# Kernel optimization log

Hardware: AMD Instinct MI355X
Metric: run time of the kernel (lower is better)

The kernel has to match this reference:

```python
import jax, jax.numpy as jnp
import numpy as np

EPS = 1e-8
NUM_ROUTING_ITERS = 3


def setup_inputs() -> dict:
    key = jax.random.key(0)
    k1, k2 = jax.random.split(key)
    x = jax.random.normal(k1, (128, 2048, 16), dtype=jnp.float32)  # [B, C, I]
    W = jax.random.normal(k2, (1, 2048, 32, 16, 16), dtype=jnp.float32)  # [1, C, J, I, U]
    return {"x": x, "W": W}


def _squash(s, axis):
    # Faithful to torch squash: dim=2 of s_j [B,1,J,U,1] is the num_units axis.
    mag_sq = jnp.sum(s * s, axis=axis, keepdims=True)
    mag = jnp.sqrt(mag_sq + EPS)
    return mag_sq / (1.0 + mag_sq) * (s / (mag + EPS))


def reference(x, W):
    # u_hat[b,c,j,u] = sum_i x[b,c,i] * W[0,c,j,i,u]
    u_hat = jnp.einsum('bci,cjiu->bcju', x, W[0])  # [B, C, J, U]
    B, C, J, U = u_hat.shape
    b_ij = jnp.zeros((B, C, J), dtype=x.dtype)
    v_j = None
    for it in range(NUM_ROUTING_ITERS):
        c_ij = jax.nn.softmax(b_ij, axis=2)                 # softmax over J (num_units)
        s_j = jnp.einsum('bcj,bcju->bju', c_ij, u_hat)      # sum over input capsules C
        # Original squashes dim=2 of [B,1,J,U,1] -> the J axis (axis=1 here).
        v_j = _squash(s_j, axis=1)                          # [B, J, U]
        if it < NUM_ROUTING_ITERS - 1:
            b_ij = b_ij + jnp.einsum('bcju,bju->bcj', u_hat, v_j)
    return v_j  # [B, J, U]
```

## Files before the change

### kernel.cpp

```cpp
#include <hip/hip_runtime.h>
#include <cstdint>
#include <cstddef>


#define CN     2048
#define JN     32
#define UN     16
#define IN_    16
#define CPB    32
#define PAIRS  (CPB/2)
#define NCHUNK (CN/CPB)
#define NBG    2

typedef _Float16 f16;
typedef _Float16 f16x2 __attribute__((ext_vector_type(2)));
typedef _Float16 f16x4 __attribute__((ext_vector_type(4)));
typedef _Float16 f16x8 __attribute__((ext_vector_type(8)));
typedef __fp16   h16x2 __attribute__((ext_vector_type(2)));
typedef float    f32x4 __attribute__((ext_vector_type(4)));

static __device__ __forceinline__ f16x2 pkrtz(float a, float b) {
    h16x2 r = __builtin_amdgcn_cvt_pkrtz(a, b);
    return __builtin_bit_cast(f16x2, r);
}
static __device__ __forceinline__ float fdot2(f16x2 a, f16x2 b, float c) {
    return __builtin_amdgcn_fdot2(__builtin_bit_cast(h16x2, a),
                                  __builtin_bit_cast(h16x2, b), c, false);
}
struct P2 { f16x2 a, b; };
static __device__ __forceinline__ f16x4 join2(f16x2 a, f16x2 b) {
    P2 p{a, b};
    return __builtin_bit_cast(f16x4, p);
}
struct P4 { f16x4 a, b; };
static __device__ __forceinline__ f16x8 join4(f16x4 a, f16x4 b) {
    P4 p{a, b};
    return __builtin_bit_cast(f16x8, p);
}
static __device__ __forceinline__ f16x8 pk8(const float* w) {
    return join4(join2(pkrtz(w[0],w[1]), pkrtz(w[2],w[3])),
                 join2(pkrtz(w[4],w[5]), pkrtz(w[6],w[7])));
}
static __device__ __forceinline__ void lds_barrier() {
    asm volatile("s_waitcnt lgkmcnt(0)" ::: "memory");
    __builtin_amdgcn_s_barrier();
}

#define TJ 328
#define TI 20
__global__ __launch_bounds__(256)
void transpose_W(const float* __restrict__ W, f16* __restrict__ Wt)
{
    __shared__ float tile[31*TJ + 15*TI + 16];
    const int c = blockIdx.x;
    const int t = threadIdx.x;
#pragma unroll
    for (int h = 0; h < 8; ++h) {
        const int o = t*4 + h*1024;
        f32x4 v = *(const f32x4*)(W + (size_t)c*8192 + o);
        const int u0 = o & 15, i = (o >> 4) & 15, j = o >> 8;
        float* dst = tile + j*TJ + i*TI + u0;
        dst[0]=v[0]; dst[1]=v[1]; dst[2]=v[2]; dst[3]=v[3];
    }
    __syncthreads();
#pragma unroll
    for (int h = 0; h < 2; ++h) {
        const int s = t + h*256;
        const int j = s >> 4, u = s & 15;
        float wv[16];
#pragma unroll
        for (int i = 0; i < 16; ++i) wv[i] = tile[j*TJ + i*TI + u];
        f16* dst = Wt + (size_t)c*8192 + j*256 + u*16;
        *(f16x8*)dst       = pk8(wv);
        *(f16x8*)(dst + 8) = pk8(wv + 8);
    }
}

template<int ROUTED>
__global__ __launch_bounds__(512)
void route_kernel(const float* __restrict__ x, const f16* __restrict__ Wt,
                  const float* __restrict__ v01g, f16* __restrict__ SP16)
{
    __shared__ f16   xs[8192];
    __shared__ float psm[2][2*8*16];

    const int tid = threadIdx.x;
    const int l   = tid & 63;
    const int jg  = tid >> 6;
    const int g   = l >> 4;
    const int m15 = l & 15;

    const int bid   = blockIdx.x;
    const int xcd   = bid & 7;
    const int k     = bid >> 3;
    const int chunk = (k >> 3) * 8 + xcd;
    const int idx   = k & 7;
    const int bg    = idx >> 2;
    const int btl   = idx & 3;

    const int bl    = btl*16 + m15;
    const int bglob = bg*64 + bl;
    const int cbase = chunk * CPB;
    const int jbase = jg * 4;
    const int ccme  = g >> 1;

    {
        const int r = tid >> 5;
        const int s = tid & 31;
        const float* src = x + ((size_t)(bg*64 + btl*16 + r)*CN + cbase + s)*IN_;
        f32x4 a = *(const f32x4*)src;
        f32x4 b = *(const f32x4*)(src + 4);
        f32x4 c = *(const f32x4*)(src + 8);
        f32x4 d = *(const f32x4*)(src + 12);
        float lo8[8] = {a[0],a[1],a[2],a[3],b[0],b[1],b[2],b[3]};
        float hi8[8] = {c[0],c[1],c[2],c[3],d[0],d[1],d[2],d[3]};
        const int byte0 = r*1024 + s*32;
        const int sw    = (r & 7) << 4;
        *(f16x8*)((char*)xs + ((byte0     ) ^ sw)) = pk8(lo8);
        *(f16x8*)((char*)xs + ((byte0 + 16) ^ sw)) = pk8(hi8);
    }

    f16x2 vfr[4][2];
    if (ROUTED) {
#pragma unroll
        for (int jj = 0; jj < 4; ++jj) {
            f32x4 vv = *(const f32x4*)(v01g + (size_t)bglob*512 + (jbase+jj)*16 + 4*g);
            vfr[jj][0] = pkrtz(vv[0], vv[1]);
            vfr[jj][1] = pkrtz(vv[2], vv[3]);
        }
    }

    f32x4 acc[4];
#pragma unroll
    for (int jj = 0; jj < 4; ++jj) acc[jj] = (f32x4){0.f,0.f,0.f,0.f};
    const f32x4 zero4 = {0.f,0.f,0.f,0.f};

    lds_barrier();

    const int xsw   = (m15 & 7) << 4;
    const int xbase = m15*1024 + ccme*32 + (g&1)*16;

    f16x8 wfr[2][4];
    f16x8 xq2[2];
    float lme2[2][4];

    auto LOADP = [&](int p) {
        const int s = p & 1;
        xq2[s] = *(const f16x8*)((const char*)xs + ((xbase + p*64) ^ xsw));
        const f16* wb = Wt + (size_t)(cbase + 2*p + ccme)*8192 + jbase*256
                        + m15*16 + (g&1)*8;
#pragma unroll
        for (int jj = 0; jj < 4; ++jj)
            wfr[s][jj] = *(const f16x8*)(wb + jj*256);
    };

    auto PHASEA = [&](int p) {
        const int s = p & 1;
        const f16x8 xq = xq2[s];
        f16x8 xz;
#pragma unroll
        for (int r = 0; r < 8; ++r) xz[r] = (f16)0.f;
        const f16x8 xb0 = (ccme == 0) ? xq : xz;
        const f16x8 xb1 = (ccme == 0) ? xz : xq;
        float summe = 0.f;
#pragma unroll
        for (int jj = 0; jj < 4; ++jj) {
            f32x4 uh0 = __builtin_amdgcn_mfma_f32_16x16x32_f16(wfr[s][jj], xb0, zero4, 0,0,0);
            float d0 = fdot2(pkrtz(uh0[0], uh0[1]), vfr[jj][0], 0.f);
            d0       = fdot2(pkrtz(uh0[2], uh0[3]), vfr[jj][1], d0);
            f32x4 uh1 = __builtin_amdgcn_mfma_f32_16x16x32_f16(wfr[s][jj], xb1, zero4, 0,0,0);
            float d1 = fdot2(pkrtz(uh1[0], uh1[1]), vfr[jj][0], 0.f);
            d1       = fdot2(pkrtz(uh1[2], uh1[3]), vfr[jj][1], d1);
            float t0 = d0 + __shfl_xor(d0, 16);
            float t1 = d1 + __shfl_xor(d1, 16);
            float sown = (ccme == 0) ? t0 : t1;
            float soth = (ccme == 0) ? t1 : t0;
            float dme  = sown + __shfl_xor(soth, 32);
            float e = __expf(dme);
            summe += e;
            lme2[s][jj] = e;
        }
        if ((l & 31) < 16)
            psm[s][(ccme*8 + jg)*16 + m15] = summe;
    };

    auto PHASEB = [&](int p, float myrden) {
        const int s = p & 1;
        const f16x8 xq = xq2[s];
#pragma unroll
        for (int jj = 0; jj < 4; ++jj) {
            f16x8 bx = xq;
            if (ROUTED) {
                const f16 hsc = (f16)(lme2[s][jj] * myrden);
#pragma unroll
                for (int r = 0; r < 8; ++r) bx[r] = xq[r] * hsc;
            }
            acc[jj] = __builtin_amdgcn_mfma_f32_16x16x32_f16(wfr[s][jj], bx, acc[jj], 0,0,0);
        }
    };

    auto RDEN = [&](int p) -> float {
        const float* pp = &psm[p & 1][ccme*128 + m15];
        float d = 0.f;
#pragma unroll
        for (int q = 0; q < 8; ++q) d += pp[q*16];
        return 1.f / d;
    };

    LOADP(0);
    LOADP(1);
    if (ROUTED) { PHASEA(0); lds_barrier(); }

#pragma unroll
    for (int p = 1; p < PAIRS; ++p) {
        float myrden = 0.f;
        if (ROUTED) myrden = RDEN(p - 1);
        PHASEB(p - 1, myrden);
        if (p + 1 < PAIRS) LOADP(p + 1);
        if (ROUTED) { PHASEA(p); lds_barrier(); }
    }
    {
        float myrden = 0.f;
        if (ROUTED) myrden = RDEN(PAIRS - 1);
        PHASEB(PAIRS - 1, myrden);
    }

    f16* dst = SP16 + (((size_t)(bg*NCHUNK + chunk))*64 + bl)*512;
#pragma unroll
    for (int jj = 0; jj < 4; ++jj) {
        f32x4 a = acc[jj];
        *(f16x4*)(dst + (jbase+jj)*16 + 4*g) =
            join2(pkrtz(a[0], a[1]), pkrtz(a[2], a[3]));
    }
}

__global__ __launch_bounds__(256)
void squash_kernel(const f16* __restrict__ SP16, float* __restrict__ v0buf,
                   float* __restrict__ v01buf, float* __restrict__ outp, int mode)
{
    __shared__ float sq[256*2];
    __shared__ float msqs[16];
    const int tid = threadIdx.x;
    const int j   = tid >> 3;
    const int uh  = tid & 7;
    const int b   = blockIdx.x;
    const int bg  = b >> 6, blb = b & 63;

    const f16* base = SP16 + ((size_t)(bg*NCHUNK)*64 + blb)*512 + j*16 + uh*2;
    float s0 = 0.f, s1 = 0.f;
#pragma unroll 8
    for (int ch = 0; ch < NCHUNK; ++ch) {
        f16x2 v = *(const f16x2*)(base + (size_t)ch * 64 * 512);
        s0 += (float)v[0];
        s1 += (float)v[1];
    }
    if (mode == 0) { s0 *= (1.f/32.f); s1 *= (1.f/32.f); }

    sq[tid*2+0] = s0*s0;
    sq[tid*2+1] = s1*s1;
    __syncthreads();
    if (tid < 16) {
        const int u = tid, uq = u >> 1, par = u & 1;
        float m = 0.f;
#pragma unroll
        for (int j2 = 0; j2 < 32; ++j2) m += sq[(j2*8 + uq)*2 + par];
        msqs[u] = m;
    }
    __syncthreads();

    const size_t idx0 = (size_t)b*512 + j*16 + uh*2;
#pragma unroll
    for (int q = 0; q < 2; ++q) {
        const float s   = q ? s1 : s0;
        const float msq = msqs[uh*2 + q];
        const float mag = sqrtf(msq + 1e-8f);
        const float v   = (msq / (1.f + msq)) * (s / (mag + 1e-8f));
        const size_t idx = idx0 + q;
        if (mode == 0)      { v0buf[idx] = v; v01buf[idx] = v; }
        else if (mode == 1) { v01buf[idx] = v0buf[idx] + v; }
        else                { outp[idx] = v; }
    }
}

extern "C" void kernel_launch(void* const* d_in, const int* in_sizes, int n_in,
                              void* d_out, int out_size, void* d_ws, size_t ws_size,
                              hipStream_t stream)
{
    const float* x = (const float*)d_in[0];
    const float* W = (const float*)d_in[1];

    f16*   Wt   = (f16*)d_ws;
    f16*   SP16 = (f16*)((char*)d_ws + (size_t)33554432);
    float* v0   = (float*)((char*)d_ws + (size_t)33554432 + 8388608);
    float* v01  = v0 + 65536;
    float* out  = (float*)d_out;

    transpose_W<<<2048, 256, 0, stream>>>(W, Wt);

    dim3 grid(512), blk(512);
    route_kernel<0><<<grid, blk, 0, stream>>>(x, Wt, nullptr, SP16);
    squash_kernel  <<<128, 256, 0, stream>>>(SP16, v0, v01, out, 0);
    route_kernel<1><<<grid, blk, 0, stream>>>(x, Wt, v01, SP16);
    squash_kernel  <<<128, 256, 0, stream>>>(SP16, v0, v01, out, 1);
    route_kernel<1><<<grid, blk, 0, stream>>>(x, Wt, v01, SP16);
    squash_kernel  <<<128, 256, 0, stream>>>(SP16, v0, v01, out, 2);
}
```

Baseline: 116.1 us.

## Pre-convert x to fp16 once, deepen W prefetch to three stages, raise MFMA priority

Adds a kernel that converts x to fp16 once, so each of the three routing passes reads half the x bytes and skips the per-pass conversion. The register prefetch of W/x fragments goes from double to triple buffering, loading two pairs ahead to hide global latency. MFMA sections are wrapped in s_setprio to favour wave scheduling there. In exchange it adds a launch and a workspace write, and the extra buffer raises register pressure, which may cut occupancy.

```diff
diff --git a/kernel.cpp b/kernel.cpp
--- a/kernel.cpp
+++ b/kernel.cpp
@@ -76,9 +76,23 @@
     }
 }
 
+__global__ __launch_bounds__(256)
+void xcvt_kernel(const float* __restrict__ x, f16* __restrict__ xh)
+{
+    const size_t i0 = ((size_t)blockIdx.x*256 + threadIdx.x) * 16;
+    f32x4 a = *(const f32x4*)(x + i0);
+    f32x4 b = *(const f32x4*)(x + i0 + 4);
+    f32x4 c = *(const f32x4*)(x + i0 + 8);
+    f32x4 d = *(const f32x4*)(x + i0 + 12);
+    float lo8[8] = {a[0],a[1],a[2],a[3],b[0],b[1],b[2],b[3]};
+    float hi8[8] = {c[0],c[1],c[2],c[3],d[0],d[1],d[2],d[3]};
+    *(f16x8*)(xh + i0)     = pk8(lo8);
+    *(f16x8*)(xh + i0 + 8) = pk8(hi8);
+}
+
 template<int ROUTED>
 __global__ __launch_bounds__(512)
-void route_kernel(const float* __restrict__ x, const f16* __restrict__ Wt,
+void route_kernel(const f16* __restrict__ xh, const f16* __restrict__ Wt,
                   const float* __restrict__ v01g, f16* __restrict__ SP16)
 {
     __shared__ f16   xs[8192];
@@ -107,17 +121,13 @@
     {
         const int r = tid >> 5;
         const int s = tid & 31;
-        const float* src = x + ((size_t)(bg*64 + btl*16 + r)*CN + cbase + s)*IN_;
-        f32x4 a = *(const f32x4*)src;
-        f32x4 b = *(const f32x4*)(src + 4);
-        f32x4 c = *(const f32x4*)(src + 8);
-        f32x4 d = *(const f32x4*)(src + 12);
-        float lo8[8] = {a[0],a[1],a[2],a[3],b[0],b[1],b[2],b[3]};
-        float hi8[8] = {c[0],c[1],c[2],c[3],d[0],d[1],d[2],d[3]};
+        const f16* src = xh + ((size_t)(bg*64 + btl*16 + r)*CN + cbase + s)*IN_;
+        f16x8 lo = *(const f16x8*)src;
+        f16x8 hi = *(const f16x8*)(src + 8);
         const int byte0 = r*1024 + s*32;
         const int sw    = (r & 7) << 4;
-        *(f16x8*)((char*)xs + ((byte0     ) ^ sw)) = pk8(lo8);
-        *(f16x8*)((char*)xs + ((byte0 + 16) ^ sw)) = pk8(hi8);
+        *(f16x8*)((char*)xs + ((byte0     ) ^ sw)) = lo;
+        *(f16x8*)((char*)xs + ((byte0 + 16) ^ sw)) = hi;
     }
 
     f16x2 vfr[4][2];
@@ -140,12 +150,12 @@
     const int xsw   = (m15 & 7) << 4;
     const int xbase = m15*1024 + ccme*32 + (g&1)*16;
 
-    f16x8 wfr[2][4];
-    f16x8 xq2[2];
+    f16x8 wfr[3][4];
+    f16x8 xq2[3];
     float lme2[2][4];
 
     auto LOADP = [&](int p) {
-        const int s = p & 1;
+        const int s = p % 3;
         xq2[s] = *(const f16x8*)((const char*)xs + ((xbase + p*64) ^ xsw));
         const f16* wb = Wt + (size_t)(cbase + 2*p + ccme)*8192 + jbase*256
                         + m15*16 + (g&1)*8;
@@ -155,7 +165,8 @@
     };
 
     auto PHASEA = [&](int p) {
-        const int s = p & 1;
+        const int s = p % 3;
+        const int t2 = p & 1;
         const f16x8 xq = xq2[s];
         f16x8 xz;
 #pragma unroll
@@ -163,6 +174,7 @@
         const f16x8 xb0 = (ccme == 0) ? xq : xz;
         const f16x8 xb1 = (ccme == 0) ? xz : xq;
         float summe = 0.f;
+        __builtin_amdgcn_s_setprio(1);
 #pragma unroll
         for (int jj = 0; jj < 4; ++jj) {
             f32x4 uh0 = __builtin_amdgcn_mfma_f32_16x16x32_f16(wfr[s][jj], xb0, zero4, 0,0,0);
@@ -178,25 +190,29 @@
             float dme  = sown + __shfl_xor(soth, 32);
             float e = __expf(dme);
             summe += e;
-            lme2[s][jj] = e;
+            lme2[t2][jj] = e;
         }
+        __builtin_amdgcn_s_setprio(0);
         if ((l & 31) < 16)
-            psm[s][(ccme*8 + jg)*16 + m15] = summe;
+            psm[t2][(ccme*8 + jg)*16 + m15] = summe;
     };
 
     auto PHASEB = [&](int p, float myrden) {
-        const int s = p & 1;
+        const int s = p % 3;
+        const int t2 = p & 1;
         const f16x8 xq = xq2[s];
+        __builtin_amdgcn_s_setprio(1);
 #pragma unroll
         for (int jj = 0; jj < 4; ++jj) {
             f16x8 bx = xq;
             if (ROUTED) {
-                const f16 hsc = (f16)(lme2[s][jj] * myrden);
+                const f16 hsc = (f16)(lme2[t2][jj] * myrden);
 #pragma unroll
                 for (int r = 0; r < 8; ++r) bx[r] = xq[r] * hsc;
             }
             acc[jj] = __builtin_amdgcn_mfma_f32_16x16x32_f16(wfr[s][jj], bx, acc[jj], 0,0,0);
         }
+        __builtin_amdgcn_s_setprio(0);
     };
 
     auto RDEN = [&](int p) -> float {
@@ -209,6 +225,7 @@
 
     LOADP(0);
     LOADP(1);
+    LOADP(2);
     if (ROUTED) { PHASEA(0); lds_barrier(); }
 
 #pragma unroll
@@ -216,7 +233,7 @@
         float myrden = 0.f;
         if (ROUTED) myrden = RDEN(p - 1);
         PHASEB(p - 1, myrden);
-        if (p + 1 < PAIRS) LOADP(p + 1);
+        if (p + 2 < PAIRS) LOADP(p + 2);
         if (ROUTED) { PHASEA(p); lds_barrier(); }
     }
     {
@@ -291,17 +308,19 @@
 
     f16*   Wt   = (f16*)d_ws;
     f16*   SP16 = (f16*)((char*)d_ws + (size_t)33554432);
-    float* v0   = (float*)((char*)d_ws + (size_t)33554432 + 8388608);
+    f16*   xh   = (f16*)((char*)d_ws + (size_t)33554432 + 8388608);
+    float* v0   = (float*)((char*)d_ws + (size_t)33554432 + 2*8388608);
     float* v01  = v0 + 65536;
     float* out  = (float*)d_out;
 
     transpose_W<<<2048, 256, 0, stream>>>(W, Wt);
+    xcvt_kernel<<<1024, 256, 0, stream>>>(x, xh);
 
     dim3 grid(512), blk(512);
-    route_kernel<0><<<grid, blk, 0, stream>>>(x, Wt, nullptr, SP16);
+    route_kernel<0><<<grid, blk, 0, stream>>>(xh, Wt, nullptr, SP16);
     squash_kernel  <<<128, 256, 0, stream>>>(SP16, v0, v01, out, 0);
-    route_kernel<1><<<grid, blk, 0, stream>>>(x, Wt, v01, SP16);
+    route_kernel<1><<<grid, blk, 0, stream>>>(xh, Wt, v01, SP16);
     squash_kernel  <<<128, 256, 0, stream>>>(SP16, v0, v01, out, 1);
-    route_kernel<1><<<grid, blk, 0, stream>>>(x, Wt, v01, SP16);
+    route_kernel<1><<<grid, blk, 0, stream>>>(xh, Wt, v01, SP16);
     squash_kernel  <<<128, 256, 0, stream>>>(SP16, v0, v01, out, 2);
 }
```

Result: no change. 118.4 us (+2.0%).

## Fuse all routing stages into one cooperative persistent kernel with grid syncs

Applied to the files above, without the earlier changes.

Replaces the seven separate launches (transpose, three route passes, three squash passes) with one cooperative mega-kernel that runs each stage as a phase separated by grid.sync. The goal is to remove per-launch overhead and inter-kernel gaps. The W transpose is reworked for 512 blocks of 512 threads, each handling 4 capsules. The kernel now needs about 41KB of shared memory and the register budget of the routing path, which may lower occupancy. Squash runs on only 128 of 512 blocks while the rest idle at the grid barrier. A fallback multi-launch path is kept in case cooperative launch is not possible.

```diff
diff --git a/kernel.cpp b/kernel.cpp
--- a/kernel.cpp
+++ b/kernel.cpp
@@ -1,7 +1,10 @@
 #include <hip/hip_runtime.h>
+#include <hip/hip_cooperative_groups.h>
 #include <cstdint>
 #include <cstddef>
 
+
+namespace cg = cooperative_groups;
 
 #define CN     2048
 #define JN     32
@@ -10,7 +13,6 @@
 #define CPB    32
 #define PAIRS  (CPB/2)
 #define NCHUNK (CN/CPB)
-#define NBG    2
 
 typedef _Float16 f16;
 typedef _Float16 f16x2 __attribute__((ext_vector_type(2)));
@@ -48,41 +50,46 @@
 
 #define TJ 328
 #define TI 20
-__global__ __launch_bounds__(256)
-void transpose_W(const float* __restrict__ W, f16* __restrict__ Wt)
-{
-    __shared__ float tile[31*TJ + 15*TI + 16];
-    const int c = blockIdx.x;
+#define T_SMEM 41936
+#define R_SMEM 18432
+
+static __device__ void transpose_phase(const float* __restrict__ W,
+                                       f16* __restrict__ Wt, char* smem, int bid)
+{
+    float* tile = (float*)smem;
     const int t = threadIdx.x;
-#pragma unroll
-    for (int h = 0; h < 8; ++h) {
-        const int o = t*4 + h*1024;
-        f32x4 v = *(const f32x4*)(W + (size_t)c*8192 + o);
-        const int u0 = o & 15, i = (o >> 4) & 15, j = o >> 8;
-        float* dst = tile + j*TJ + i*TI + u0;
-        dst[0]=v[0]; dst[1]=v[1]; dst[2]=v[2]; dst[3]=v[3];
-    }
-    __syncthreads();
-#pragma unroll
-    for (int h = 0; h < 2; ++h) {
-        const int s = t + h*256;
-        const int j = s >> 4, u = s & 15;
-        float wv[16];
-#pragma unroll
-        for (int i = 0; i < 16; ++i) wv[i] = tile[j*TJ + i*TI + u];
-        f16* dst = Wt + (size_t)c*8192 + j*256 + u*16;
-        *(f16x8*)dst       = pk8(wv);
-        *(f16x8*)(dst + 8) = pk8(wv + 8);
-    }
-}
-
-template<int ROUTED>
-__global__ __launch_bounds__(512)
-void route_kernel(const float* __restrict__ x, const f16* __restrict__ Wt,
-                  const float* __restrict__ v01g, f16* __restrict__ SP16)
-{
-    __shared__ f16   xs[8192];
-    __shared__ float psm[2][2*8*16];
+    for (int cc = 0; cc < 4; ++cc) {
+        const int c = bid*4 + cc;
+#pragma unroll
+        for (int h = 0; h < 4; ++h) {
+            const int o = t*4 + h*2048;
+            f32x4 v = *(const f32x4*)(W + (size_t)c*8192 + o);
+            const int u0 = o & 15, i = (o >> 4) & 15, j = o >> 8;
+            float* dst = tile + j*TJ + i*TI + u0;
+            dst[0]=v[0]; dst[1]=v[1]; dst[2]=v[2]; dst[3]=v[3];
+        }
+        __syncthreads();
+        {
+            const int j = t >> 4, u = t & 15;
+            float wv[16];
+#pragma unroll
+            for (int i = 0; i < 16; ++i) wv[i] = tile[j*TJ + i*TI + u];
+            f16* dst = Wt + (size_t)c*8192 + j*256 + u*16;
+            *(f16x8*)dst       = pk8(wv);
+            *(f16x8*)(dst + 8) = pk8(wv + 8);
+        }
+        __syncthreads();
+    }
+}
+
+static __device__ void route_phase(const float* __restrict__ x,
+                                   const f16* __restrict__ Wt,
+                                   const float* __restrict__ v01g,
+                                   f16* __restrict__ SP16,
+                                   char* smem, bool routed, int bid)
+{
+    f16*   xs  = (f16*)smem;
+    float* psm = (float*)(smem + 16384);
 
     const int tid = threadIdx.x;
     const int l   = tid & 63;
@@ -90,7 +97,6 @@
     const int g   = l >> 4;
     const int m15 = l & 15;
 
-    const int bid   = blockIdx.x;
     const int xcd   = bid & 7;
     const int k     = bid >> 3;
     const int chunk = (k >> 3) * 8 + xcd;
@@ -121,7 +127,7 @@
     }
 
     f16x2 vfr[4][2];
-    if (ROUTED) {
+    if (routed) {
 #pragma unroll
         for (int jj = 0; jj < 4; ++jj) {
             f32x4 vv = *(const f32x4*)(v01g + (size_t)bglob*512 + (jbase+jj)*16 + 4*g);
@@ -181,7 +187,7 @@
             lme2[s][jj] = e;
         }
         if ((l & 31) < 16)
-            psm[s][(ccme*8 + jg)*16 + m15] = summe;
+            psm[(s*2 + ccme)*128 + jg*16 + m15] = summe;
     };
 
     auto PHASEB = [&](int p, float myrden) {
@@ -190,7 +196,7 @@
 #pragma unroll
         for (int jj = 0; jj < 4; ++jj) {
             f16x8 bx = xq;
-            if (ROUTED) {
+            if (routed) {
                 const f16 hsc = (f16)(lme2[s][jj] * myrden);
 #pragma unroll
                 for (int r = 0; r < 8; ++r) bx[r] = xq[r] * hsc;
@@ -200,7 +206,7 @@
     };
 
     auto RDEN = [&](int p) -> float {
-        const float* pp = &psm[p & 1][ccme*128 + m15];
+        const float* pp = &psm[((p & 1)*2 + ccme)*128 + m15];
         float d = 0.f;
 #pragma unroll
         for (int q = 0; q < 8; ++q) d += pp[q*16];
@@ -209,19 +215,17 @@
 
     LOADP(0);
     LOADP(1);
-    if (ROUTED) { PHASEA(0); lds_barrier(); }
+    if (routed) { PHASEA(0); lds_barrier(); }
 
 #pragma unroll
     for (int p = 1; p < PAIRS; ++p) {
-        float myrden = 0.f;
-        if (ROUTED) myrden = RDEN(p - 1);
+        float myrden = routed ? RDEN(p - 1) : 0.f;
         PHASEB(p - 1, myrden);
         if (p + 1 < PAIRS) LOADP(p + 1);
-        if (ROUTED) { PHASEA(p); lds_barrier(); }
+        if (routed) { PHASEA(p); lds_barrier(); }
     }
     {
-        float myrden = 0.f;
-        if (ROUTED) myrden = RDEN(PAIRS - 1);
+        float myrden = routed ? RDEN(PAIRS - 1) : 0.f;
         PHASEB(PAIRS - 1, myrden);
     }
 
@@ -234,30 +238,35 @@
     }
 }
 
-__global__ __launch_bounds__(256)
-void squash_kernel(const f16* __restrict__ SP16, float* __restrict__ v0buf,
-                   float* __restrict__ v01buf, float* __restrict__ outp, int mode)
-{
-    __shared__ float sq[256*2];
-    __shared__ float msqs[16];
+static __device__ void squash_phase(const f16* __restrict__ SP16,
+                                    float* __restrict__ v0buf,
+                                    float* __restrict__ v01buf,
+                                    float* __restrict__ outp,
+                                    int mode, char* smem, int bid)
+{
+    if (bid >= 128) return;
+    float* sq   = (float*)smem;
+    float* msqs = sq + 512;
     const int tid = threadIdx.x;
-    const int j   = tid >> 3;
-    const int uh  = tid & 7;
-    const int b   = blockIdx.x;
+    const int b   = bid;
     const int bg  = b >> 6, blb = b & 63;
 
-    const f16* base = SP16 + ((size_t)(bg*NCHUNK)*64 + blb)*512 + j*16 + uh*2;
     float s0 = 0.f, s1 = 0.f;
+    int j = 0, uh = 0;
+    if (tid < 256) {
+        j  = tid >> 3;
+        uh = tid & 7;
+        const f16* base = SP16 + ((size_t)(bg*NCHUNK)*64 + blb)*512 + j*16 + uh*2;
 #pragma unroll 8
-    for (int ch = 0; ch < NCHUNK; ++ch) {
-        f16x2 v = *(const f16x2*)(base + (size_t)ch * 64 * 512);
-        s0 += (float)v[0];
-        s1 += (float)v[1];
-    }
-    if (mode == 0) { s0 *= (1.f/32.f); s1 *= (1.f/32.f); }
-
-    sq[tid*2+0] = s0*s0;
-    sq[tid*2+1] = s1*s1;
+        for (int ch = 0; ch < NCHUNK; ++ch) {
+            f16x2 v = *(const f16x2*)(base + (size_t)ch * 64 * 512);
+            s0 += (float)v[0];
+            s1 += (float)v[1];
+        }
+        if (mode == 0) { s0 *= (1.f/32.f); s1 *= (1.f/32.f); }
+        sq[tid*2+0] = s0*s0;
+        sq[tid*2+1] = s1*s1;
+    }
     __syncthreads();
     if (tid < 16) {
         const int u = tid, uq = u >> 1, par = u & 1;
@@ -267,19 +276,70 @@
         msqs[u] = m;
     }
     __syncthreads();
-
-    const size_t idx0 = (size_t)b*512 + j*16 + uh*2;
-#pragma unroll
-    for (int q = 0; q < 2; ++q) {
-        const float s   = q ? s1 : s0;
-        const float msq = msqs[uh*2 + q];
-        const float mag = sqrtf(msq + 1e-8f);
-        const float v   = (msq / (1.f + msq)) * (s / (mag + 1e-8f));
-        const size_t idx = idx0 + q;
-        if (mode == 0)      { v0buf[idx] = v; v01buf[idx] = v; }
-        else if (mode == 1) { v01buf[idx] = v0buf[idx] + v; }
-        else                { outp[idx] = v; }
-    }
+    if (tid < 256) {
+        const size_t idx0 = (size_t)b*512 + j*16 + uh*2;
+#pragma unroll
+        for (int q = 0; q < 2; ++q) {
+            const float s   = q ? s1 : s0;
+            const float msq = msqs[uh*2 + q];
+            const float mag = sqrtf(msq + 1e-8f);
+            const float v   = (msq / (1.f + msq)) * (s / (mag + 1e-8f));
+            const size_t idx = idx0 + q;
+            if (mode == 0)      { v0buf[idx] = v; v01buf[idx] = v; }
+            else if (mode == 1) { v01buf[idx] = v0buf[idx] + v; }
+            else                { outp[idx] = v; }
+        }
+    }
+}
+
+__global__ __launch_bounds__(512)
+void mega_kernel(const float* __restrict__ x, const float* __restrict__ W,
+                 f16* __restrict__ Wt, f16* __restrict__ SP16,
+                 float* __restrict__ v0, float* __restrict__ v01,
+                 float* __restrict__ out)
+{
+    cg::grid_group grid = cg::this_grid();
+    __shared__ alignas(16) char smem[T_SMEM];
+    const int bid = blockIdx.x;
+
+    transpose_phase(W, Wt, smem, bid);
+    __threadfence(); grid.sync();
+
+    route_phase(x, Wt, nullptr, SP16, smem, false, bid);
+    __threadfence(); grid.sync();
+    squash_phase(SP16, v0, v01, out, 0, smem, bid);
+    __threadfence(); grid.sync();
+
+    route_phase(x, Wt, v01, SP16, smem, true, bid);
+    __threadfence(); grid.sync();
+    squash_phase(SP16, v0, v01, out, 1, smem, bid);
+    __threadfence(); grid.sync();
+
+    route_phase(x, Wt, v01, SP16, smem, true, bid);
+    __threadfence(); grid.sync();
+    squash_phase(SP16, v0, v01, out, 2, smem, bid);
+}
+
+__global__ __launch_bounds__(512)
+void transpose_k(const float* __restrict__ W, f16* __restrict__ Wt)
+{
+    __shared__ alignas(16) char smem[T_SMEM];
+    transpose_phase(W, Wt, smem, blockIdx.x);
+}
+template<int ROUTED>
+__global__ __launch_bounds__(512)
+void route_k(const float* __restrict__ x, const f16* __restrict__ Wt,
+             const float* __restrict__ v01g, f16* __restrict__ SP16)
+{
+    __shared__ alignas(16) char smem[R_SMEM];
+    route_phase(x, Wt, v01g, SP16, smem, ROUTED != 0, blockIdx.x);
+}
+__global__ __launch_bounds__(512)
+void squash_k(const f16* __restrict__ SP16, float* __restrict__ v0,
+              float* __restrict__ v01, float* __restrict__ out, int mode)
+{
+    __shared__ alignas(16) char smem[2112 + 16];
+    squash_phase(SP16, v0, v01, out, mode, smem, blockIdx.x);
 }
 
 extern "C" void kernel_launch(void* const* d_in, const int* in_sizes, int n_in,
@@ -295,13 +355,23 @@
     float* v01  = v0 + 65536;
     float* out  = (float*)d_out;
 
-    transpose_W<<<2048, 256, 0, stream>>>(W, Wt);
-
-    dim3 grid(512), blk(512);
-    route_kernel<0><<<grid, blk, 0, stream>>>(x, Wt, nullptr, SP16);
-    squash_kernel  <<<128, 256, 0, stream>>>(SP16, v0, v01, out, 0);
-    route_kernel<1><<<grid, blk, 0, stream>>>(x, Wt, v01, SP16);
-    squash_kernel  <<<128, 256, 0, stream>>>(SP16, v0, v01, out, 1);
-    route_kernel<1><<<grid, blk, 0, stream>>>(x, Wt, v01, SP16);
-    squash_kernel  <<<128, 256, 0, stream>>>(SP16, v0, v01, out, 2);
-}
+    int occ = 0;
+    hipError_t qe = hipOccupancyMaxActiveBlocksPerMultiprocessor(
+        &occ, reinterpret_cast<const void*>(mega_kernel), 512, 0);
+    const bool coop = (qe == hipSuccess) && (occ * 256 >= 512);
+
+    if (coop) {
+        void* args[] = { (void*)&x, (void*)&W, (void*)&Wt, (void*)&SP16,
+                         (void*)&v0, (void*)&v01, (void*)&out };
+        hipLaunchCooperativeKernel((void*)mega_kernel, dim3(512), dim3(512),
+                                   args, 0, stream);
+    } else {
+        transpose_k<<<512, 512, 0, stream>>>(W, Wt);
+        route_k<0> <<<512, 512, 0, stream>>>(x, Wt, nullptr, SP16);
+        squash_k   <<<128, 512, 0, stream>>>(SP16, v0, v01, out, 0);
+        route_k<1> <<<512, 512, 0, stream>>>(x, Wt, v01, SP16);
+        squash_k   <<<128, 512, 0, stream>>>(SP16, v0, v01, out, 1);
+        route_k<1> <<<512, 512, 0, stream>>>(x, Wt, v01, SP16);
+        squash_k   <<<128, 512, 0, stream>>>(SP16, v0, v01, out, 2);
+    }
+}
```

Measured after the change: 154.6 us. +33.2%, slower.
